# Performance work log

Measured on AMD Instinct MI355X. Metric: run time of the kernel, lower is better.

The kernel has to match this reference:

```python
import jax, jax.numpy as jnp
import numpy as np

N_NODES = 50000
N_EDGES = 800000
IN_CH = 128
OUT_CH = 128
LN_EPS = 1e-5


def setup_inputs() -> dict:
    key = jax.random.key(0)
    k1, k2, k3, k4 = jax.random.split(key, 4)
    x = jax.random.normal(k1, (N_NODES, IN_CH), dtype=jnp.float32)
    edge_index = jax.random.randint(k2, (2, N_EDGES), 0, N_NODES, dtype=jnp.int64)
    # GCNConv linear weight (glorot-ish scale) and bias
    W = jax.random.normal(k3, (IN_CH, OUT_CH), dtype=jnp.float32) * (1.0 / np.sqrt(IN_CH))
    b = jnp.zeros((OUT_CH,), dtype=jnp.float32)
    # LayerNorm affine params
    ln_w = jnp.ones((OUT_CH,), dtype=jnp.float32)
    ln_b = jnp.zeros((OUT_CH,), dtype=jnp.float32)
    del k4
    return {"x": x, "edge_index": edge_index, "W": W, "b": b, "ln_w": ln_w, "ln_b": ln_b}


def reference(x, edge_index, W, b, ln_w, ln_b):
    N = x.shape[0]
    # --- GCNConv: add self loops, symmetric normalization, scatter-add ---
    loop = jnp.arange(N, dtype=edge_index.dtype)
    row = jnp.concatenate([edge_index[0], loop])  # source nodes (x_j)
    col = jnp.concatenate([edge_index[1], loop])  # target nodes (aggregate here)
    h = x @ W  # [N, out]
    deg = jax.ops.segment_sum(jnp.ones(row.shape[0], dtype=h.dtype), col, num_segments=N)
    dinv = jnp.where(deg > 0, jax.lax.rsqrt(deg), 0.0)
    norm = dinv[row] * dinv[col]  # [E+N]
    msg = h[row] * norm[:, None]  # gather + scale
    out = jax.ops.segment_sum(msg, col, num_segments=N) + b  # scatter-add + bias
    # --- LayerNorm over feature dim ---
    mu = jnp.mean(out, axis=-1, keepdims=True)
    var = jnp.mean(jnp.square(out - mu), axis=-1, keepdims=True)
    out = (out - mu) * jax.lax.rsqrt(var + LN_EPS) * ln_w + ln_b
    # --- ReLU; dropout is identity in eval mode ---
    return jax.nn.relu(out)
```

## Files before the change

kernel.cpp:

```cpp
#include <hip/hip_runtime.h>
#include <hip/hip_bf16.h>

#define CH 128
#define LN_EPS 1e-5f
#define PBITS 8
#define CAP 8192

typedef unsigned int uint;
typedef unsigned short ushort;
typedef __attribute__((ext_vector_type(8))) short short8;
typedef __attribute__((ext_vector_type(4))) float f32x4;

__device__ __forceinline__ float bflo(uint v) { return __uint_as_float(v << 16); }
__device__ __forceinline__ float bfhi(uint v) { return __uint_as_float(v & 0xffff0000u); }
__device__ __forceinline__ ushort f2bf(float f) {
    uint u = __float_as_uint(f);
    u += 0x7fffu + ((u >> 16) & 1u);
    return (ushort)(u >> 16);
}

__global__ __launch_bounds__(256) void k_bucket(const int* __restrict__ row,
                                                const int* __restrict__ col,
                                                uint* __restrict__ bk,
                                                uint* __restrict__ bcur,
                                                int E, int NB) {
    __shared__ uint cnt[256], startl[256], basel[256], wtot[4];
    __shared__ uint sortv[4096];
    __shared__ int  dstg[4096];
    const int t = threadIdx.x, lane = t & 63, w = t >> 6;
    const int cs = blockIdx.x * 4096;
    const int m = min(4096, E - cs);

    cnt[t] = 0;
    __syncthreads();

    int  eb[16]; int erl[16]; uint ev[16];
#pragma unroll
    for (int k = 0; k < 16; ++k) {
        int i = t + k * 256;
        eb[k] = -1;
        if (i < m) {
            int c = col[cs + i];
            int r = row[cs + i];
            eb[k]  = c >> PBITS;
            ev[k]  = ((uint)(c & 255) << 16) | (uint)r;
            erl[k] = (int)atomicAdd(&cnt[eb[k]], 1u);
        }
    }
    __syncthreads();

    uint c0 = cnt[t];
    if (t < NB && c0) basel[t] = atomicAdd(&bcur[t], c0);
    uint s = c0;
#pragma unroll
    for (int d = 1; d < 64; d <<= 1) { uint v = __shfl_up(s, d); if (lane >= d) s += v; }
    if (lane == 63) wtot[w] = s;
    __syncthreads();
    uint pre = 0;
    for (int j = 0; j < w; ++j) pre += wtot[j];
    startl[t] = pre + s - c0;
    __syncthreads();

#pragma unroll
    for (int k = 0; k < 16; ++k) {
        if (eb[k] >= 0) {
            int pos = (int)startl[eb[k]] + erl[k];
            sortv[pos] = ev[k];
            dstg[pos]  = eb[k] * CAP + (int)basel[eb[k]] + erl[k];
        }
    }
    __syncthreads();

#pragma unroll
    for (int k = 0; k < 16; ++k) {
        int i = t + k * 256;
        if (i < m) bk[dstg[i]] = sortv[i];
    }
}

__global__ __launch_bounds__(256) void k_csr(const uint* __restrict__ bk,
                                             const uint* __restrict__ bcur,
                                             int* __restrict__ csr,
                                             int* __restrict__ deg,
                                             int* __restrict__ offs,
                                             float* __restrict__ dinv, int N) {
    __shared__ uint hist[256], startl[256], wtot[4];
    __shared__ ushort rls[CAP];
    const int t = threadIdx.x, lane = t & 63, w = t >> 6;
    const int b = blockIdx.x;
    const int base = b * CAP;
    const int cntb = (int)bcur[b];

    hist[t] = 0;
    __syncthreads();

    for (int i = t; i < cntb; i += 256) {
        uint v = bk[base + i];
        rls[i] = (ushort)atomicAdd(&hist[v >> 16], 1u);
    }
    __syncthreads();

    uint c0 = hist[t];
    uint s = c0;
#pragma unroll
    for (int d = 1; d < 64; d <<= 1) { uint v = __shfl_up(s, d); if (lane >= d) s += v; }
    if (lane == 63) wtot[w] = s;
    __syncthreads();
    uint pre = 0;
    for (int j = 0; j < w; ++j) pre += wtot[j];
    startl[t] = pre + s - c0;

    int node = (b << PBITS) + t;
    if (node < N) {
        deg[node]  = (int)c0;
        offs[node] = base + (int)(pre + s - c0);
        dinv[node] = rsqrtf((float)c0 + 1.0f);
    }
    __syncthreads();

    for (int i = t; i < cntb; i += 256) {
        uint v = bk[base + i];
        csr[base + (int)startl[v >> 16] + (int)rls[i]] = (int)(v & 0xffffu);
    }
}

__global__ void k_wt(const float* __restrict__ W, ushort* __restrict__ Wt) {
    int o = blockIdx.x * 256 + threadIdx.x;
    int c = o >> 7, k = o & 127;
    Wt[o] = f2bf(W[k * CH + c]);
}

__global__ __launch_bounds__(256) void k_gemm(const float* __restrict__ x,
                                              const ushort* __restrict__ Wt,
                                              ushort* __restrict__ h, int N) {
    __shared__ __align__(16) ushort xs[64 * 128];
    __shared__ __align__(16) ushort ws[128 * 128];
    const int t  = threadIdx.x;
    const int bm = blockIdx.x * 64;

#pragma unroll
    for (int i = 0; i < 8; ++i) {
        int gi = t + i * 256;
        int c = gi >> 4, g = gi & 15;
        uint4 v = *reinterpret_cast<const uint4*>(&Wt[gi * 8]);
        *reinterpret_cast<uint4*>(&ws[c * 128 + ((g ^ (c & 7)) << 3)]) = v;
    }
#pragma unroll
    for (int i = 0; i < 4; ++i) {
        int gi = t + i * 256;
        int r = gi >> 4, g = gi & 15;
        int row = bm + r;
        uint4 p = make_uint4(0u, 0u, 0u, 0u);
        if (row < N) {
            float4 va = *reinterpret_cast<const float4*>(&x[(size_t)row * CH + g * 8]);
            float4 vb = *reinterpret_cast<const float4*>(&x[(size_t)row * CH + g * 8 + 4]);
            p.x = ((uint)f2bf(va.y) << 16) | f2bf(va.x);
            p.y = ((uint)f2bf(va.w) << 16) | f2bf(va.z);
            p.z = ((uint)f2bf(vb.y) << 16) | f2bf(vb.x);
            p.w = ((uint)f2bf(vb.w) << 16) | f2bf(vb.z);
        }
        *reinterpret_cast<uint4*>(&xs[r * 128 + ((g ^ (r & 7)) << 3)]) = p;
    }
    __syncthreads();

    const int w  = t >> 6, l = t & 63;
    const int lr = l & 15;
    const int kg = l >> 4;
    f32x4 acc[8] = {};

#pragma unroll
    for (int s = 0; s < 4; ++s) {
        int g  = s * 4 + kg;
        int ar = w * 16 + lr;
        short8 a = *reinterpret_cast<const short8*>(&xs[ar * 128 + ((g ^ (ar & 7)) << 3)]);
#pragma unroll
        for (int c = 0; c < 8; ++c) {
            int bc = c * 16 + lr;
            short8 b = *reinterpret_cast<const short8*>(&ws[bc * 128 + ((g ^ (bc & 7)) << 3)]);
            acc[c] = __builtin_amdgcn_mfma_f32_16x16x32_bf16(a, b, acc[c], 0, 0, 0);
        }
    }

#pragma unroll
    for (int c = 0; c < 8; ++c)
#pragma unroll
        for (int j = 0; j < 4; ++j) {
            int row = bm + w * 16 + kg * 4 + j;
            if (row < N) h[(size_t)row * CH + c * 16 + lr] = f2bf(acc[c][j]);
        }
}

__global__ __launch_bounds__(256) void k_agg(const uint2* __restrict__ hu2,
                                             const int* __restrict__ offs,
                                             const int* __restrict__ deg,
                                             const float* __restrict__ dinv,
                                             const int* __restrict__ csr,
                                             const float* __restrict__ bias,
                                             const float* __restrict__ lnw,
                                             const float* __restrict__ lnb,
                                             float* __restrict__ out, int N) {
    const int wave = threadIdx.x >> 6;
    const int lane = threadIdx.x & 63;
    const int half = lane >> 5;
    const int li   = lane & 31;
    const int n = blockIdx.x * 4 + wave;
    if (n >= N) return;

    const float di = dinv[n];
    const int start = offs[n];
    const int cnt = deg[n];

    float ax = 0.f, ay = 0.f, az = 0.f, aw = 0.f;
    if (half == 0) {
        uint2 sv = hu2[((size_t)n << 5) + li];
        float w = di * di;
        ax = bflo(sv.x) * w; ay = bfhi(sv.x) * w;
        az = bflo(sv.y) * w; aw = bfhi(sv.y) * w;
    }

    for (int base = 0; base < cnt; base += 64) {
        int m = cnt - base; if (m > 64) m = 64;
        int idx = 0; float dv = 0.f;
        if (lane < m) {
            idx = csr[start + base + lane];
            dv  = dinv[idx] * di;
        }
        for (int j = 0; j < m; j += 8) {
            int j0 = j + half;
            int   s0 = __shfl(idx, j0),     s1 = __shfl(idx, j0 + 2);
            int   s2 = __shfl(idx, j0 + 4), s3 = __shfl(idx, j0 + 6);
            float w0 = __shfl(dv, j0),      w1 = __shfl(dv, j0 + 2);
            float w2 = __shfl(dv, j0 + 4),  w3 = __shfl(dv, j0 + 6);
            uint2 v0 = hu2[((size_t)s0 << 5) + li];
            uint2 v1 = hu2[((size_t)s1 << 5) + li];
            uint2 v2 = hu2[((size_t)s2 << 5) + li];
            uint2 v3 = hu2[((size_t)s3 << 5) + li];
            ax = fmaf(bflo(v0.x), w0, ax); ay = fmaf(bfhi(v0.x), w0, ay);
            az = fmaf(bflo(v0.y), w0, az); aw = fmaf(bfhi(v0.y), w0, aw);
            ax = fmaf(bflo(v1.x), w1, ax); ay = fmaf(bfhi(v1.x), w1, ay);
            az = fmaf(bflo(v1.y), w1, az); aw = fmaf(bfhi(v1.y), w1, aw);
            ax = fmaf(bflo(v2.x), w2, ax); ay = fmaf(bfhi(v2.x), w2, ay);
            az = fmaf(bflo(v2.y), w2, az); aw = fmaf(bfhi(v2.y), w2, aw);
            ax = fmaf(bflo(v3.x), w3, ax); ay = fmaf(bfhi(v3.x), w3, ay);
            az = fmaf(bflo(v3.y), w3, az); aw = fmaf(bfhi(v3.y), w3, aw);
        }
    }

    ax += __shfl_xor(ax, 32); ay += __shfl_xor(ay, 32);
    az += __shfl_xor(az, 32); aw += __shfl_xor(aw, 32);

    float4 bb = reinterpret_cast<const float4*>(bias)[li];
    ax += bb.x; ay += bb.y; az += bb.z; aw += bb.w;

    float sum = ax + ay + az + aw;
    float sq  = ax * ax + ay * ay + az * az + aw * aw;
#pragma unroll
    for (int d = 16; d >= 1; d >>= 1) {
        sum += __shfl_xor(sum, d);
        sq  += __shfl_xor(sq, d);
    }
    float mean = sum * (1.0f / 128.0f);
    float var  = sq * (1.0f / 128.0f) - mean * mean;
    float rstd = rsqrtf(var + LN_EPS);

    if (half == 0) {
        float4 w4 = reinterpret_cast<const float4*>(lnw)[li];
        float4 b4 = reinterpret_cast<const float4*>(lnb)[li];
        float4 y;
        y.x = fmaxf((ax - mean) * rstd * w4.x + b4.x, 0.f);
        y.y = fmaxf((ay - mean) * rstd * w4.y + b4.y, 0.f);
        y.z = fmaxf((az - mean) * rstd * w4.z + b4.z, 0.f);
        y.w = fmaxf((aw - mean) * rstd * w4.w + b4.w, 0.f);
        reinterpret_cast<float4*>(out)[((size_t)n << 5) + li] = y;
    }
}

extern "C" void kernel_launch(void* const* d_in, const int* in_sizes, int n_in,
                              void* d_out, int out_size, void* d_ws, size_t ws_size,
                              hipStream_t stream) {
    const float* x   = (const float*)d_in[0];
    const int*   ei  = (const int*)d_in[1];
    const float* W   = (const float*)d_in[2];
    const float* b   = (const float*)d_in[3];
    const float* lnw = (const float*)d_in[4];
    const float* lnb = (const float*)d_in[5];
    float* out = (float*)d_out;

    const int N = in_sizes[0] / CH;
    const int E = in_sizes[1] / 2;
    const int NB = (N + 255) >> PBITS;
    const int* row = ei;
    const int* col = ei + E;

    char* w8 = (char*)d_ws;
    ushort* h    = (ushort*)w8;
    int*   deg   = (int*)(w8 + (size_t)N * CH * 2);
    int*   offs  = deg + N;
    float* dinv  = (float*)(offs + N);
    uint*  bcur  = (uint*)(dinv + N);
    uint*  bk    = bcur + 256;
    int*   csr   = (int*)(bk + (size_t)NB * CAP);
    ushort* Wt   = (ushort*)(csr + (size_t)NB * CAP);

    hipMemsetAsync(bcur, 0, 256 * sizeof(uint), stream);

    k_bucket<<<(E + 4095) / 4096, 256, 0, stream>>>(row, col, bk, bcur, E, NB);

    k_wt<<<CH * CH / 256, 256, 0, stream>>>(W, Wt);

    k_gemm<<<(N + 63) / 64, 256, 0, stream>>>(x, Wt, h, N);

    k_csr<<<NB, 256, 0, stream>>>(bk, bcur, csr, deg, offs, dinv, N);

    k_agg<<<(N + 3) / 4, 256, 0, stream>>>((const uint2*)h, offs, deg, dinv, csr,
                                           b, lnw, lnb, out, N);
}
```

Measured before the change: 82.60 us.

## Fuse edge bucketing with GEMM in one launch and fold memset into transpose

Merges the edge-bucketing kernel and the bf16 MFMA GEMM into one kernel. Blocks below NBK do bucketing and the remaining blocks do GEMM tiles, so the two independent stages run concurrently. The bcur memset is moved into the W-transpose init kernel, which cuts the launch count from five (plus a memset) to four. The cost is a shared 48KB LDS footprint for the bucketing blocks, which may reduce their occupancy.

Result: faster. 71.37 us (-13.6%).

```diff
diff --git a/kernel.cpp b/kernel.cpp
--- a/kernel.cpp
+++ b/kernel.cpp
@@ -19,62 +19,136 @@
     return (ushort)(u >> 16);
 }
 
-__global__ __launch_bounds__(256) void k_bucket(const int* __restrict__ row,
-                                                const int* __restrict__ col,
-                                                uint* __restrict__ bk,
-                                                uint* __restrict__ bcur,
-                                                int E, int NB) {
-    __shared__ uint cnt[256], startl[256], basel[256], wtot[4];
-    __shared__ uint sortv[4096];
-    __shared__ int  dstg[4096];
-    const int t = threadIdx.x, lane = t & 63, w = t >> 6;
-    const int cs = blockIdx.x * 4096;
-    const int m = min(4096, E - cs);
-
-    cnt[t] = 0;
-    __syncthreads();
-
-    int  eb[16]; int erl[16]; uint ev[16];
-#pragma unroll
-    for (int k = 0; k < 16; ++k) {
-        int i = t + k * 256;
-        eb[k] = -1;
-        if (i < m) {
-            int c = col[cs + i];
-            int r = row[cs + i];
-            eb[k]  = c >> PBITS;
-            ev[k]  = ((uint)(c & 255) << 16) | (uint)r;
-            erl[k] = (int)atomicAdd(&cnt[eb[k]], 1u);
-        }
-    }
-    __syncthreads();
-
-    uint c0 = cnt[t];
-    if (t < NB && c0) basel[t] = atomicAdd(&bcur[t], c0);
-    uint s = c0;
-#pragma unroll
-    for (int d = 1; d < 64; d <<= 1) { uint v = __shfl_up(s, d); if (lane >= d) s += v; }
-    if (lane == 63) wtot[w] = s;
-    __syncthreads();
-    uint pre = 0;
-    for (int j = 0; j < w; ++j) pre += wtot[j];
-    startl[t] = pre + s - c0;
-    __syncthreads();
-
-#pragma unroll
-    for (int k = 0; k < 16; ++k) {
-        if (eb[k] >= 0) {
-            int pos = (int)startl[eb[k]] + erl[k];
-            sortv[pos] = ev[k];
-            dstg[pos]  = eb[k] * CAP + (int)basel[eb[k]] + erl[k];
-        }
-    }
-    __syncthreads();
-
-#pragma unroll
-    for (int k = 0; k < 16; ++k) {
-        int i = t + k * 256;
-        if (i < m) bk[dstg[i]] = sortv[i];
+__global__ void k_init(const float* __restrict__ W, ushort* __restrict__ Wt,
+                       uint* __restrict__ bcur) {
+    if (blockIdx.x == 0) bcur[threadIdx.x] = 0;
+    int o = blockIdx.x * 256 + threadIdx.x;
+    int c = o >> 7, k = o & 127;
+    Wt[o] = f2bf(W[k * CH + c]);
+}
+
+__global__ __launch_bounds__(256) void k_fused(const int* __restrict__ row,
+                                               const int* __restrict__ col,
+                                               uint* __restrict__ bk,
+                                               uint* __restrict__ bcur,
+                                               int E, int NB, int NBK,
+                                               const float* __restrict__ x,
+                                               const ushort* __restrict__ Wt,
+                                               ushort* __restrict__ h, int N) {
+    __shared__ __align__(16) char smem[49152];
+    const int t = threadIdx.x;
+
+    if ((int)blockIdx.x < NBK) {
+        uint* cnt    = (uint*)smem;
+        uint* startl = cnt + 256;
+        uint* basel  = startl + 256;
+        uint* wtot   = basel + 256;
+        uint* sortv  = wtot + 4;
+        int*  dstg   = (int*)(sortv + 4096);
+        const int lane = t & 63, w = t >> 6;
+        const int cs = blockIdx.x * 4096;
+        const int m = min(4096, E - cs);
+
+        cnt[t] = 0;
+        __syncthreads();
+
+        int  eb[16]; int erl[16]; uint ev[16];
+#pragma unroll
+        for (int k = 0; k < 16; ++k) {
+            int i = t + k * 256;
+            eb[k] = -1;
+            if (i < m) {
+                int c = col[cs + i];
+                int r = row[cs + i];
+                eb[k]  = c >> PBITS;
+                ev[k]  = ((uint)(c & 255) << 16) | (uint)r;
+                erl[k] = (int)atomicAdd(&cnt[eb[k]], 1u);
+            }
+        }
+        __syncthreads();
+
+        uint c0 = cnt[t];
+        if (t < NB && c0) basel[t] = atomicAdd(&bcur[t], c0);
+        uint s = c0;
+#pragma unroll
+        for (int d = 1; d < 64; d <<= 1) { uint v = __shfl_up(s, d); if (lane >= d) s += v; }
+        if (lane == 63) wtot[w] = s;
+        __syncthreads();
+        uint pre = 0;
+        for (int j = 0; j < w; ++j) pre += wtot[j];
+        startl[t] = pre + s - c0;
+        __syncthreads();
+
+#pragma unroll
+        for (int k = 0; k < 16; ++k) {
+            if (eb[k] >= 0) {
+                int pos = (int)startl[eb[k]] + erl[k];
+                sortv[pos] = ev[k];
+                dstg[pos]  = eb[k] * CAP + (int)basel[eb[k]] + erl[k];
+            }
+        }
+        __syncthreads();
+
+#pragma unroll
+        for (int k = 0; k < 16; ++k) {
+            int i = t + k * 256;
+            if (i < m) bk[dstg[i]] = sortv[i];
+        }
+    } else {
+        ushort* xs = (ushort*)smem;
+        ushort* ws = xs + 64 * 128;
+        const int bm = ((int)blockIdx.x - NBK) * 64;
+
+#pragma unroll
+        for (int i = 0; i < 8; ++i) {
+            int gi = t + i * 256;
+            int c = gi >> 4, g = gi & 15;
+            uint4 v = *reinterpret_cast<const uint4*>(&Wt[gi * 8]);
+            *reinterpret_cast<uint4*>(&ws[c * 128 + ((g ^ (c & 7)) << 3)]) = v;
+        }
+#pragma unroll
+        for (int i = 0; i < 4; ++i) {
+            int gi = t + i * 256;
+            int r = gi >> 4, g = gi & 15;
+            int rw = bm + r;
+            uint4 p = make_uint4(0u, 0u, 0u, 0u);
+            if (rw < N) {
+                float4 va = *reinterpret_cast<const float4*>(&x[(size_t)rw * CH + g * 8]);
+                float4 vb = *reinterpret_cast<const float4*>(&x[(size_t)rw * CH + g * 8 + 4]);
+                p.x = ((uint)f2bf(va.y) << 16) | f2bf(va.x);
+                p.y = ((uint)f2bf(va.w) << 16) | f2bf(va.z);
+                p.z = ((uint)f2bf(vb.y) << 16) | f2bf(vb.x);
+                p.w = ((uint)f2bf(vb.w) << 16) | f2bf(vb.z);
+            }
+            *reinterpret_cast<uint4*>(&xs[r * 128 + ((g ^ (r & 7)) << 3)]) = p;
+        }
+        __syncthreads();
+
+        const int w  = t >> 6, l = t & 63;
+        const int lr = l & 15;
+        const int kg = l >> 4;
+        f32x4 acc[8] = {};
+
+#pragma unroll
+        for (int s = 0; s < 4; ++s) {
+            int g  = s * 4 + kg;
+            int ar = w * 16 + lr;
+            short8 a = *reinterpret_cast<const short8*>(&xs[ar * 128 + ((g ^ (ar & 7)) << 3)]);
+#pragma unroll
+            for (int c = 0; c < 8; ++c) {
+                int bc = c * 16 + lr;
+                short8 b = *reinterpret_cast<const short8*>(&ws[bc * 128 + ((g ^ (bc & 7)) << 3)]);
+                acc[c] = __builtin_amdgcn_mfma_f32_16x16x32_bf16(a, b, acc[c], 0, 0, 0);
+            }
+        }
+
+#pragma unroll
+        for (int c = 0; c < 8; ++c)
+#pragma unroll
+            for (int j = 0; j < 4; ++j) {
+                int rw = bm + w * 16 + kg * 4 + j;
+                if (rw < N) h[(size_t)rw * CH + c * 16 + lr] = f2bf(acc[c][j]);
+            }
     }
 }
 
@@ -122,72 +196,6 @@
         uint v = bk[base + i];
         csr[base + (int)startl[v >> 16] + (int)rls[i]] = (int)(v & 0xffffu);
     }
-}
-
-__global__ void k_wt(const float* __restrict__ W, ushort* __restrict__ Wt) {
-    int o = blockIdx.x * 256 + threadIdx.x;
-    int c = o >> 7, k = o & 127;
-    Wt[o] = f2bf(W[k * CH + c]);
-}
-
-__global__ __launch_bounds__(256) void k_gemm(const float* __restrict__ x,
-                                              const ushort* __restrict__ Wt,
-                                              ushort* __restrict__ h, int N) {
-    __shared__ __align__(16) ushort xs[64 * 128];
-    __shared__ __align__(16) ushort ws[128 * 128];
-    const int t  = threadIdx.x;
-    const int bm = blockIdx.x * 64;
-
-#pragma unroll
-    for (int i = 0; i < 8; ++i) {
-        int gi = t + i * 256;
-        int c = gi >> 4, g = gi & 15;
-        uint4 v = *reinterpret_cast<const uint4*>(&Wt[gi * 8]);
-        *reinterpret_cast<uint4*>(&ws[c * 128 + ((g ^ (c & 7)) << 3)]) = v;
-    }
-#pragma unroll
-    for (int i = 0; i < 4; ++i) {
-        int gi = t + i * 256;
-        int r = gi >> 4, g = gi & 15;
-        int row = bm + r;
-        uint4 p = make_uint4(0u, 0u, 0u, 0u);
-        if (row < N) {
-            float4 va = *reinterpret_cast<const float4*>(&x[(size_t)row * CH + g * 8]);
-            float4 vb = *reinterpret_cast<const float4*>(&x[(size_t)row * CH + g * 8 + 4]);
-            p.x = ((uint)f2bf(va.y) << 16) | f2bf(va.x);
-            p.y = ((uint)f2bf(va.w) << 16) | f2bf(va.z);
-            p.z = ((uint)f2bf(vb.y) << 16) | f2bf(vb.x);
-            p.w = ((uint)f2bf(vb.w) << 16) | f2bf(vb.z);
-        }
-        *reinterpret_cast<uint4*>(&xs[r * 128 + ((g ^ (r & 7)) << 3)]) = p;
-    }
-    __syncthreads();
-
-    const int w  = t >> 6, l = t & 63;
-    const int lr = l & 15;
-    const int kg = l >> 4;
-    f32x4 acc[8] = {};
-
-#pragma unroll
-    for (int s = 0; s < 4; ++s) {
-        int g  = s * 4 + kg;
-        int ar = w * 16 + lr;
-        short8 a = *reinterpret_cast<const short8*>(&xs[ar * 128 + ((g ^ (ar & 7)) << 3)]);
-#pragma unroll
-        for (int c = 0; c < 8; ++c) {
-            int bc = c * 16 + lr;
-            short8 b = *reinterpret_cast<const short8*>(&ws[bc * 128 + ((g ^ (bc & 7)) << 3)]);
-            acc[c] = __builtin_amdgcn_mfma_f32_16x16x32_bf16(a, b, acc[c], 0, 0, 0);
-        }
-    }
-
-#pragma unroll
-    for (int c = 0; c < 8; ++c)
-#pragma unroll
-        for (int j = 0; j < 4; ++j) {
-            int row = bm + w * 16 + kg * 4 + j;
-            if (row < N) h[(size_t)row * CH + c * 16 + lr] = f2bf(acc[c][j]);
-        }
 }
 
 __global__ __launch_bounds__(256) void k_agg(const uint2* __restrict__ hu2,
@@ -288,7 +296,9 @@
 
     const int N = in_sizes[0] / CH;
     const int E = in_sizes[1] / 2;
-    const int NB = (N + 255) >> PBITS;
+    const int NB  = (N + 255) >> PBITS;
+    const int NBK = (E + 4095) / 4096;
+    const int NG  = (N + 63) / 64;
     const int* row = ei;
     const int* col = ei + E;
 
@@ -302,13 +312,10 @@
     int*   csr   = (int*)(bk + (size_t)NB * CAP);
     ushort* Wt   = (ushort*)(csr + (size_t)NB * CAP);
 
-    hipMemsetAsync(bcur, 0, 256 * sizeof(uint), stream);
-
-    k_bucket<<<(E + 4095) / 4096, 256, 0, stream>>>(row, col, bk, bcur, E, NB);
-
-    k_wt<<<CH * CH / 256, 256, 0, stream>>>(W, Wt);
-
-    k_gemm<<<(N + 63) / 64, 256, 0, stream>>>(x, Wt, h, N);
+    k_init<<<CH * CH / 256, 256, 0, stream>>>(W, Wt, bcur);
+
+    k_fused<<<NBK + NG, 256, 0, stream>>>(row, col, bk, bcur, E, NB, NBK,
+                                          x, Wt, h, N);
 
     k_csr<<<NB, 256, 0, stream>>>(bk, bcur, csr, deg, offs, dinv, N);
 
```
